# Optimization experiments

Measured on AMD Instinct MI355X. Metric: run time of the kernel, lower is better.

The kernel has to match this reference:

```python
import jax, jax.numpy as jnp
import numpy as np

S, B, V, D, H, G = 60, 256, 50000, 300, 512, 15  # seq, batch, vocab, embed/proj, hidden, grid
DM, DOUT = 1024, 2
MLP_IN = G * G + 7  # 225 pooled + 7 extra features = 232


def setup_inputs() -> dict:
    key = jax.random.key(0)
    ks = jax.random.split(key, 16)
    n = lambda k, shp: (jax.random.normal(k, shp, jnp.float32) * 0.02)
    return {
        "embed_table": n(ks[0], (V, D)),
        "proj_W": n(ks[1], (D, D)),
        "proj_b": jnp.zeros((D,), jnp.float32),
        "bn_g": jnp.ones((D,), jnp.float32),
        "bn_b": jnp.zeros((D,), jnp.float32),
        "Wih": n(ks[2], (4 * H, D)),
        "Whh": n(ks[3], (4 * H, H)),
        "bih": jnp.zeros((4 * H,), jnp.float32),
        "bhh": jnp.zeros((4 * H,), jnp.float32),
        "W1": n(ks[4], (DM, MLP_IN)),
        "b1": jnp.zeros((DM,), jnp.float32),
        "g1": jnp.ones((DM,), jnp.float32),
        "be1": jnp.zeros((DM,), jnp.float32),
        "W2": n(ks[5], (DM, DM)),
        "b2": jnp.zeros((DM,), jnp.float32),
        "g2": jnp.ones((DM,), jnp.float32),
        "be2": jnp.zeros((DM,), jnp.float32),
        "W3": n(ks[6], (DOUT, DM)),
        "b3": jnp.zeros((DOUT,), jnp.float32),
        "extra_feats": jax.random.normal(ks[7], (B, 7), jnp.float32),
        "sentence1": jax.random.randint(ks[8], (S, B), 0, V, jnp.int32),
        "sentence2": jax.random.randint(ks[9], (S, B), 0, V, jnp.int32),
    }


def _bn(x, g, b, axes):
    mu = x.mean(axis=axes, keepdims=True)
    var = x.var(axis=axes, keepdims=True)
    return (x - mu) * jax.lax.rsqrt(var + 1e-5) * g + b


def reference(embed_table, proj_W, proj_b, bn_g, bn_b, Wih, Whh, bih, bhh,
              W1, b1, g1, be1, W2, b2, g2, be2, W3, b3,
              extra_feats, sentence1, sentence2):
    def encode(tokens):
        e = embed_table[tokens]                      # [S,B,D] gather
        e = e @ proj_W.T + proj_b                    # Bottle Linear over S*B rows
        e = _bn(e, bn_g, bn_b, (0, 1))               # Bottle BatchNorm over S*B rows

        def step(carry, x):
            h, c = carry
            z = x @ Wih.T + h @ Whh.T + (bih + bhh)  # [B,4H], gate order i,f,g,o
            i, f, g_, o = jnp.split(z, 4, axis=-1)
            c = jax.nn.sigmoid(f) * c + jax.nn.sigmoid(i) * jnp.tanh(g_)
            h = jax.nn.sigmoid(o) * jnp.tanh(c)
            return (h, c), h

        init = (jnp.zeros((B, H), e.dtype), jnp.zeros((B, H), e.dtype))
        _, hs = jax.lax.scan(step, init, e)          # [S,B,H]
        return hs.transpose(1, 0, 2)                 # [B,S,H]

    h1 = encode(sentence1)
    h2 = encode(sentence2)

    # pairwise L2 distance matrix per batch element: [B,S,S]
    sq = (jnp.sum(h1 * h1, -1)[:, :, None]
          + jnp.sum(h2 * h2, -1)[:, None, :]
          - 2.0 * jnp.einsum('bid,bjd->bij', h1, h2))
    dist = jnp.sqrt(jnp.maximum(sq, 0.0) + 1e-12)

    # dynamic 15x15 min-pool (S divisible by G => kernel = S//G)
    k = S // G
    pooled = dist.reshape(B, G, k, G, k).min(axis=(2, 4)).reshape(B, G * G)

    x = jnp.concatenate([pooled, extra_feats], axis=1)  # [B,232]
    x = _bn(jax.nn.relu(x @ W1.T + b1), g1, be1, (0,))
    x = _bn(jax.nn.relu(x @ W2.T + b2), g2, be2, (0,))
    return jax.nn.log_softmax(x @ W3.T + b3, axis=-1)   # [B,2]
```

## Files before the change

### kernel.cpp

```cpp
#include <hip/hip_runtime.h>
#include <hip/hip_bf16.h>

#define S_LEN 60
#define BATCH 256
#define EMB   300
#define EMBP  320
#define HID   512
#define DMLP  1024
#define NROW  (2*S_LEN*BATCH)
#define RPS   (S_LEN*BATCH)

typedef __attribute__((ext_vector_type(8))) short short8v;
typedef __attribute__((ext_vector_type(4))) float f32x4;

static __device__ __forceinline__ float sigf(float x){
  return 1.0f/(1.0f+__expf(-x));
}
static __device__ __forceinline__ float tanh_fast(float x){
  x = fminf(fmaxf(x,-40.0f),40.0f);
  float a = __expf(2.0f*x);
  return (a-1.0f)/(a+1.0f);
}
static __device__ __forceinline__ unsigned short f2b(float v){
  __hip_bfloat16 h = __float2bfloat16(v);
  return *(unsigned short*)&h;
}
static __device__ __forceinline__ float b2f(unsigned short u){
  return __uint_as_float(((unsigned int)u)<<16);
}

__global__ __launch_bounds__(256) void k_conv_weights(
    const float* __restrict__ Wih, const float* __restrict__ Whh,
    const float* __restrict__ bih, const float* __restrict__ bhh,
    const float* __restrict__ projW,
    unsigned short* __restrict__ Wihb, unsigned short* __restrict__ Whhb,
    unsigned short* __restrict__ projWb, float* __restrict__ bsum)
{
  const int tid = blockIdx.x*256 + threadIdx.x;
  const int stride = gridDim.x*256;
  for (int i=tid; i<2048*EMBP; i+=stride){
    int n = i/EMBP, k = i - n*EMBP;
    Wihb[i] = f2b((k<EMB) ? Wih[(size_t)n*EMB + k] : 0.0f);
  }
  for (int i=tid; i<2048*HID; i+=stride) Whhb[i] = f2b(Whh[i]);
  for (int i=tid; i<EMBP*EMBP; i+=stride){
    int n = i/EMBP, k = i - n*EMBP;
    projWb[i] = f2b((n<EMB && k<EMB) ? projW[(size_t)n*EMB + k] : 0.0f);
  }
  for (int i=tid; i<2048; i+=stride) bsum[i] = bih[i]+bhh[i];
}

__global__ __launch_bounds__(512) void k_embed_mfma(
    const float* __restrict__ embed, const unsigned short* __restrict__ projWb,
    const float* __restrict__ projb, const int* __restrict__ s1,
    const int* __restrict__ s2, unsigned short* __restrict__ Pb)
{
  __shared__ __align__(16) unsigned short sA0[64*40];
  __shared__ __align__(16) unsigned short sA1[64*40];
  __shared__ __align__(16) unsigned short sW0[64*40];
  __shared__ __align__(16) unsigned short sW1[64*40];
  __shared__ int stok[64];
  const int m0 = blockIdx.x*64, n0 = blockIdx.y*64;
  const int tid = threadIdx.x;
  if (tid < 64){
    int r = m0 + tid;
    stok[tid] = (r < RPS) ? s1[r] : s2[r-RPS];
  }
  __syncthreads();
  const int lane = tid & 63, w = tid>>6;
  const int wr = w>>2, wc = w&3;
  const bool isA = tid < 256;
  const int srow = (tid&255)>>2, sseg = tid&3;
  const float* Arow = embed + (size_t)stok[srow]*EMB;
  const unsigned short* Wrow = projWb + (size_t)(n0+srow)*EMBP;

  const int ldst = srow*40 + sseg*8;
  const int aoff0 = (wr*32 + (lane&15))*40 + (lane>>4)*8;
  const int aoff1 = aoff0 + 16*40;
  const int woff  = (wc*16 + (lane&15))*40 + (lane>>4)*8;

  f32x4 acc0 = {0.f,0.f,0.f,0.f}, acc1 = {0.f,0.f,0.f,0.f};

  auto loadA = [&](int kk)->uint4 {
    int kb = kk*32 + sseg*8;
    unsigned short t8[8];
    if (kb+7 < EMB){
      float4 f0 = *(const float4*)(Arow + kb);
      float4 f1 = *(const float4*)(Arow + kb + 4);
      t8[0]=f2b(f0.x); t8[1]=f2b(f0.y); t8[2]=f2b(f0.z); t8[3]=f2b(f0.w);
      t8[4]=f2b(f1.x); t8[5]=f2b(f1.y); t8[6]=f2b(f1.z); t8[7]=f2b(f1.w);
    } else {
      #pragma unroll
      for (int jq=0; jq<8; jq++){
        int k = kb+jq;
        t8[jq] = f2b((k<EMB) ? Arow[k] : 0.0f);
      }
    }
    uint4 o;
    o.x = (unsigned)t8[0] | ((unsigned)t8[1]<<16);
    o.y = (unsigned)t8[2] | ((unsigned)t8[3]<<16);
    o.z = (unsigned)t8[4] | ((unsigned)t8[5]<<16);
    o.w = (unsigned)t8[6] | ((unsigned)t8[7]<<16);
    return o;
  };

  if (isA) *(uint4*)(sA0 + ldst) = loadA(0);
  else     *(uint4*)(sW0 + ldst) = *(const uint4*)(Wrow + sseg*8);
  __syncthreads();

  for (int kk=0; kk<10; kk++){
    uint4 nv;
    if (kk < 9){
      if (isA) nv = loadA(kk+1);
      else     nv = *(const uint4*)(Wrow + (kk+1)*32 + sseg*8);
    }
    const unsigned short* A = (kk&1) ? sA1 : sA0;
    const unsigned short* W = (kk&1) ? sW1 : sW0;
    short8v af0 = *(const short8v*)(A + aoff0);
    short8v af1 = *(const short8v*)(A + aoff1);
    short8v wf  = *(const short8v*)(W + woff);
    acc0 = __builtin_amdgcn_mfma_f32_16x16x32_bf16(af0, wf, acc0, 0,0,0);
    acc1 = __builtin_amdgcn_mfma_f32_16x16x32_bf16(af1, wf, acc1, 0,0,0);
    if (kk < 9){
      unsigned short* dst = ((kk&1) ? (isA?sA0:sW0) : (isA?sA1:sW1)) + ldst;
      *(uint4*)dst = nv;
    }
    __syncthreads();
  }

  const int cc = wc*16 + (lane&15);
  const int n = n0 + cc;
  const float bias = (n < EMB) ? projb[n] : 0.0f;
  const bool valid = (n < EMB);
  #pragma unroll
  for (int v=0; v<4; v++){
    int r0 = wr*32 + (lane>>4)*4 + v;
    Pb[(size_t)(m0+r0)*EMBP + n]    = f2b(valid ? acc0[v]+bias : 0.0f);
    Pb[(size_t)(m0+r0+16)*EMBP + n] = f2b(valid ? acc1[v]+bias : 0.0f);
  }
}

__global__ __launch_bounds__(320) void k_bn_partial(const unsigned short* __restrict__ Pb,
    float* __restrict__ ps, float* __restrict__ psq)
{
  const int rb = blockIdx.x, sent = blockIdx.y, t = threadIdx.x;
  if (t >= EMB) return;
  const unsigned short* base = Pb + ((size_t)sent*RPS + (size_t)rb*256)*EMBP;
  float s=0.0f, q=0.0f;
  for (int r=0;r<256;r++){
    float v = b2f(base[(size_t)r*EMBP + t]);
    s += v; q = fmaf(v,v,q);
  }
  ps [(size_t)(sent*60+rb)*EMB + t] = s;
  psq[(size_t)(sent*60+rb)*EMB + t] = q;
}

__global__ __launch_bounds__(320) void k_bn_final(const float* __restrict__ ps,
    const float* __restrict__ psq, const float* __restrict__ g,
    const float* __restrict__ b, float* __restrict__ scale, float* __restrict__ shift)
{
  const int sent = blockIdx.x, t = threadIdx.x;
  if (t >= EMB) return;
  float s=0.0f, q=0.0f;
  for (int i=0;i<60;i++){
    s += ps [(size_t)(sent*60+i)*EMB + t];
    q += psq[(size_t)(sent*60+i)*EMB + t];
  }
  float mean = s * (1.0f/15360.0f);
  float var  = q * (1.0f/15360.0f) - mean*mean;
  float sc = g[t] * rsqrtf(var + 1e-5f);
  scale[sent*EMB+t] = sc;
  shift[sent*EMB+t] = b[t] - mean*sc;
}

__global__ __launch_bounds__(256) void k_bn_apply(unsigned short* __restrict__ Pb,
    const float* __restrict__ scale, const float* __restrict__ shift)
{
  const int r = blockIdx.x*8 + (threadIdx.x>>5);
  const int c0 = threadIdx.x & 31;
  const int sent = (r >= RPS) ? 1 : 0;
  unsigned short* row = Pb + (size_t)r*EMBP;
  for (int c=c0; c<EMB; c+=32){
    float v = b2f(row[c]);
    v = fmaf(v, scale[sent*EMB+c], shift[sent*EMB+c]);
    row[c] = f2b(v);
  }
}

__global__ __launch_bounds__(512) void k_lstm_step(
    const unsigned short* __restrict__ Pb,
    const unsigned short* __restrict__ Wihb,
    const unsigned short* __restrict__ Whhb,
    const float* __restrict__ bsum,
    const unsigned short* __restrict__ Hin,
    unsigned short* __restrict__ Hnext,
    float* __restrict__ cst,
    unsigned short* __restrict__ Hout,
    int tstep)
{
  __shared__ __align__(16) unsigned short smem[4*5120];
  float* zs = (float*)smem;

  const int tid = threadIdx.x;
  const int lane = tid & 63, w = tid >> 6;
  const int wr = w >> 2, wc = w & 3;
  const int j0 = (int)blockIdx.x * 16;
  const int m0 = (int)blockIdx.y * 64;
  const int sent = m0 >> 8;
  const int brow = m0 & 255;

  const int half = tid >> 8;
  const int rs = tid & 255;
  const int srow = rs >> 2, sseg = rs & 3;
  const int kb = half*32 + sseg*8;
  const int ldst = half*2560 + srow*40 + sseg*8;

  const unsigned short* pAx = Pb + ((size_t)((sent*S_LEN + tstep)*BATCH) + brow + srow)*EMBP + kb;
  const unsigned short* pAh = Hin + (size_t)(m0 + srow)*HID + kb;
  const int wn = (srow>>4)*HID + j0 + (srow&15);
  const unsigned short* pWx = Wihb + (size_t)wn*EMBP + kb;
  const unsigned short* pWh = Whhb + (size_t)wn*HID  + kb;

  auto loadA = [&](int c)->uint4 {
    return (c < 5) ? *(const uint4*)(pAx + c*64) : *(const uint4*)(pAh + (c-5)*64);
  };
  auto loadW = [&](int c)->uint4 {
    return (c < 5) ? *(const uint4*)(pWx + c*64) : *(const uint4*)(pWh + (c-5)*64);
  };

  const int aoffB = (wr*32 + (lane&15))*40 + (lane>>4)*8;
  const int woffB = (wc*16 + (lane&15))*40 + (lane>>4)*8;

  f32x4 acc0 = {0.f,0.f,0.f,0.f}, acc1 = {0.f,0.f,0.f,0.f};

  uint4 rA[3], rW[3];
  rA[0] = loadA(0); rW[0] = loadW(0);
  rA[1] = loadA(1); rW[1] = loadW(1);
  rA[2] = loadA(2); rW[2] = loadW(2);
  *(uint4*)(smem + ldst)         = rA[0];
  *(uint4*)(smem + 10240 + ldst) = rW[0];
  __syncthreads();

  #pragma unroll
  for (int kk = 0; kk < 13; kk++){
    if (kk + 3 < 13){
      rA[(kk+3)%3] = loadA(kk+3);
      rW[(kk+3)%3] = loadW(kk+3);
    }
    const unsigned short* A = smem + (kk&1)*5120;
    const unsigned short* W = smem + 10240 + (kk&1)*5120;
    #pragma unroll
    for (int h2 = 0; h2 < 2; h2++){
      const int bh = h2*2560;
      short8v wf = *(const short8v*)(W + bh + woffB);
      short8v a0 = *(const short8v*)(A + bh + aoffB);
      short8v a1 = *(const short8v*)(A + bh + aoffB + 16*40);
      acc0 = __builtin_amdgcn_mfma_f32_16x16x32_bf16(a0, wf, acc0, 0,0,0);
      acc1 = __builtin_amdgcn_mfma_f32_16x16x32_bf16(a1, wf, acc1, 0,0,0);
    }
    if (kk + 1 < 13){
      *(uint4*)(smem + ((kk+1)&1)*5120 + ldst)         = rA[(kk+1)%3];
      *(uint4*)(smem + 10240 + ((kk+1)&1)*5120 + ldst) = rW[(kk+1)%3];
    }
    __syncthreads();
  }

  #pragma unroll
  for (int v = 0; v < 4; v++){
    int r0 = wr*32 + (lane>>4)*4 + v;
    int cc = wc*16 + (lane&15);
    zs[r0*66 + cc]      = acc0[v];
    zs[(r0+16)*66 + cc] = acc1[v];
  }
  __syncthreads();

  const int row_e = tid >> 4, jj = tid & 15, j = j0 + jj;
  const float zb0 = bsum[0*HID+j], zb1 = bsum[1*HID+j];
  const float zb2 = bsum[2*HID+j], zb3 = bsum[3*HID+j];
  #pragma unroll
  for (int q = 0; q < 2; q++){
    int row = row_e + q*32;
    int r = m0 + row;
    float zi = zs[row*66 + jj]    + zb0;
    float zf = zs[row*66 + 16+jj] + zb1;
    float zg = zs[row*66 + 32+jj] + zb2;
    float zo = zs[row*66 + 48+jj] + zb3;
    size_t ci = (size_t)r*HID + j;
    float cn = fmaf(sigf(zf), cst[ci], sigf(zi)*tanh_fast(zg));
    cst[ci] = cn;
    float hn = sigf(zo)*tanh_fast(cn);
    unsigned short hb = f2b(hn);
    Hnext[ci] = hb;
    Hout[((size_t)((sent*S_LEN + tstep)*BATCH) + (r&255))*HID + j] = hb;
  }
}

#define SDU 258
__global__ __launch_bounds__(256) void k_dist_pool(
    const unsigned short* __restrict__ Hout, float* __restrict__ pooled)
{
  __shared__ unsigned int h1s[S_LEN*SDU];
  __shared__ unsigned int h2s[S_LEN*SDU];
  __shared__ float n1s[S_LEN], n2s[S_LEN];
  const int b = blockIdx.x, tid = threadIdx.x;
  const unsigned int* H = (const unsigned int*)Hout;
  for (int e=tid; e<S_LEN*256; e+=256){
    int row = e>>8, cu = e&255;
    h1s[row*SDU+cu] = H[((size_t)(0*S_LEN+row)*BATCH + b)*256 + cu];
    h2s[row*SDU+cu] = H[((size_t)(1*S_LEN+row)*BATCH + b)*256 + cu];
  }
  __syncthreads();
  if (tid < S_LEN){
    const unsigned int* rp = &h1s[tid*SDU];
    float q=0.0f;
    for (int cu=0;cu<256;cu++){
      unsigned int u = rp[cu];
      float lo = __uint_as_float(u<<16);
      float hi = __uint_as_float(u & 0xffff0000u);
      q = fmaf(lo,lo,q); q = fmaf(hi,hi,q);
    }
    n1s[tid] = q;
  } else if (tid >= 64 && tid < 64+S_LEN){
    const unsigned int* rp = &h2s[(tid-64)*SDU];
    float q=0.0f;
    for (int cu=0;cu<256;cu++){
      unsigned int u = rp[cu];
      float lo = __uint_as_float(u<<16);
      float hi = __uint_as_float(u & 0xffff0000u);
      q = fmaf(lo,lo,q); q = fmaf(hi,hi,q);
    }
    n2s[tid-64] = q;
  }
  __syncthreads();
  if (tid < 225){
    const int gi = tid/15, gj = tid%15;
    float acc[4][4];
    #pragma unroll
    for (int a=0;a<4;a++)
      #pragma unroll
      for (int c=0;c<4;c++) acc[a][c]=0.0f;
    const unsigned int* r1[4]; const unsigned int* r2[4];
    #pragma unroll
    for (int a=0;a<4;a++){ r1[a]=&h1s[(gi*4+a)*SDU]; r2[a]=&h2s[(gj*4+a)*SDU]; }
    for (int cu=0;cu<256;cu++){
      float lo1[4],hi1[4],lo2[4],hi2[4];
      #pragma unroll
      for (int a=0;a<4;a++){
        unsigned int u = r1[a][cu];
        lo1[a]=__uint_as_float(u<<16); hi1[a]=__uint_as_float(u&0xffff0000u);
      }
      #pragma unroll
      for (int c=0;c<4;c++){
        unsigned int u = r2[c][cu];
        lo2[c]=__uint_as_float(u<<16); hi2[c]=__uint_as_float(u&0xffff0000u);
      }
      #pragma unroll
      for (int a=0;a<4;a++)
        #pragma unroll
        for (int c=0;c<4;c++)
          acc[a][c] = fmaf(lo1[a],lo2[c], fmaf(hi1[a],hi2[c], acc[a][c]));
    }
    float mn = 3.4e38f;
    #pragma unroll
    for (int a=0;a<4;a++)
      #pragma unroll
      for (int c=0;c<4;c++){
        float sq = n1s[gi*4+a] + n2s[gj*4+c] - 2.0f*acc[a][c];
        mn = fminf(mn, sqrtf(fmaxf(sq,0.0f)+1e-12f));
      }
    pooled[(size_t)b*225 + tid] = mn;
  }
}

__global__ __launch_bounds__(256) void k_mlp1(const float* __restrict__ pooled,
    const float* __restrict__ extra, const float* __restrict__ W1,
    const float* __restrict__ b1, float* __restrict__ y1)
{
  __shared__ __align__(16) float xs[232];
  const int b = blockIdx.x, tid = threadIdx.x;
  if (tid < 225) xs[tid] = pooled[(size_t)b*225 + tid];
  else if (tid < 232) xs[tid] = extra[(size_t)b*7 + (tid-225)];
  __syncthreads();
  #pragma unroll
  for (int q=0;q<4;q++){
    int n = tid + q*256;
    float acc = b1[n];
    const float4* wr = (const float4*)(W1 + (size_t)n*232);
    const float4* xr = (const float4*)xs;
    for (int k4=0;k4<58;k4++){
      float4 w = wr[k4]; float4 x = xr[k4];
      acc = fmaf(w.x,x.x, fmaf(w.y,x.y, fmaf(w.z,x.z, fmaf(w.w,x.w, acc))));
    }
    y1[(size_t)b*DMLP + n] = fmaxf(acc, 0.0f);
  }
}

__global__ __launch_bounds__(256) void k_mlp_bn(const float* __restrict__ y,
    const float* __restrict__ g, const float* __restrict__ be,
    float* __restrict__ scale, float* __restrict__ shift)
{
  const int n = blockIdx.x*256 + threadIdx.x;
  float s=0.0f, q=0.0f;
  for (int b=0;b<BATCH;b++){
    float v = y[(size_t)b*DMLP + n];
    s += v; q = fmaf(v,v,q);
  }
  float mean = s * (1.0f/256.0f);
  float var  = q * (1.0f/256.0f) - mean*mean;
  float sc = g[n] * rsqrtf(var + 1e-5f);
  scale[n] = sc;
  shift[n] = be[n] - mean*sc;
}

__global__ __launch_bounds__(256) void k_mlp2(const float* __restrict__ y1,
    const float* __restrict__ scale1, const float* __restrict__ shift1,
    const float* __restrict__ W2, const float* __restrict__ b2,
    float* __restrict__ y2)
{
  __shared__ __align__(16) float xs[4][DMLP];
  const int b0 = blockIdx.x*4, tid = threadIdx.x;
  for (int e=tid; e<4*DMLP; e+=256){
    int bb = e>>10, k = e&1023;
    xs[bb][k] = fmaf(y1[(size_t)(b0+bb)*DMLP + k], scale1[k], shift1[k]);
  }
  __syncthreads();
  #pragma unroll
  for (int q=0;q<4;q++){
    int n = tid + q*256;
    float a0=0.0f,a1=0.0f,a2=0.0f,a3=0.0f;
    const float4* wr = (const float4*)(W2 + (size_t)n*DMLP);
    for (int k4=0;k4<256;k4++){
      float4 w = wr[k4];
      float4 x0 = ((const float4*)xs[0])[k4];
      float4 x1 = ((const float4*)xs[1])[k4];
      float4 x2 = ((const float4*)xs[2])[k4];
      float4 x3 = ((const float4*)xs[3])[k4];
      a0 = fmaf(w.x,x0.x, fmaf(w.y,x0.y, fmaf(w.z,x0.z, fmaf(w.w,x0.w, a0))));
      a1 = fmaf(w.x,x1.x, fmaf(w.y,x1.y, fmaf(w.z,x1.z, fmaf(w.w,x1.w, a1))));
      a2 = fmaf(w.x,x2.x, fmaf(w.y,x2.y, fmaf(w.z,x2.z, fmaf(w.w,x2.w, a2))));
      a3 = fmaf(w.x,x3.x, fmaf(w.y,x3.y, fmaf(w.z,x3.z, fmaf(w.w,x3.w, a3))));
    }
    float bias = b2[n];
    y2[(size_t)(b0+0)*DMLP + n] = fmaxf(a0+bias, 0.0f);
    y2[(size_t)(b0+1)*DMLP + n] = fmaxf(a1+bias, 0.0f);
    y2[(size_t)(b0+2)*DMLP + n] = fmaxf(a2+bias, 0.0f);
    y2[(size_t)(b0+3)*DMLP + n] = fmaxf(a3+bias, 0.0f);
  }
}

__global__ __launch_bounds__(256) void k_mlp3(const float* __restrict__ y2,
    const float* __restrict__ scale2, const float* __restrict__ shift2,
    const float* __restrict__ W3, const float* __restrict__ b3,
    float* __restrict__ out)
{
  __shared__ float r0[256], r1[256];
  const int b = blockIdx.x, tid = threadIdx.x;
  float p0=0.0f, p1=0.0f;
  #pragma unroll
  for (int q=0;q<4;q++){
    int k = tid + q*256;
    float x = fmaf(y2[(size_t)b*DMLP + k], scale2[k], shift2[k]);
    p0 = fmaf(x, W3[k], p0);
    p1 = fmaf(x, W3[DMLP+k], p1);
  }
  r0[tid]=p0; r1[tid]=p1;
  __syncthreads();
  for (int s=128; s>0; s>>=1){
    if (tid<s){ r0[tid]+=r0[tid+s]; r1[tid]+=r1[tid+s]; }
    __syncthreads();
  }
  if (tid==0){
    float l0 = r0[0]+b3[0], l1 = r1[0]+b3[1];
    float m = fmaxf(l0,l1);
    float lse = m + logf(__expf(l0-m)+__expf(l1-m));
    out[b*2+0] = l0-lse;
    out[b*2+1] = l1-lse;
  }
}

extern "C" void kernel_launch(void* const* d_in, const int* in_sizes, int n_in,
                              void* d_out, int out_size, void* d_ws, size_t ws_size,
                              hipStream_t stream)
{
  (void)in_sizes; (void)n_in; (void)out_size; (void)ws_size;
  const float* embed = (const float*)d_in[0];
  const float* projW = (const float*)d_in[1];
  const float* projb = (const float*)d_in[2];
  const float* bn_g  = (const float*)d_in[3];
  const float* bn_b  = (const float*)d_in[4];
  const float* Wih   = (const float*)d_in[5];
  const float* Whh   = (const float*)d_in[6];
  const float* bih   = (const float*)d_in[7];
  const float* bhh   = (const float*)d_in[8];
  const float* W1    = (const float*)d_in[9];
  const float* b1    = (const float*)d_in[10];
  const float* g1    = (const float*)d_in[11];
  const float* be1   = (const float*)d_in[12];
  const float* W2    = (const float*)d_in[13];
  const float* b2    = (const float*)d_in[14];
  const float* g2    = (const float*)d_in[15];
  const float* be2   = (const float*)d_in[16];
  const float* W3    = (const float*)d_in[17];
  const float* b3    = (const float*)d_in[18];
  const float* extra = (const float*)d_in[19];
  const int*   s1    = (const int*)d_in[20];
  const int*   s2    = (const int*)d_in[21];
  float* out = (float*)d_out;

  float* ws = (float*)d_ws;
  size_t off = 0;
  float* ps   = ws + off; off += (size_t)2*60*EMB;
  float* psq  = ws + off; off += (size_t)2*60*EMB;
  float* bnsc = ws + off; off += 2*EMB;
  float* bnsh = ws + off; off += 2*EMB;
  float* bsum = ws + off; off += 2048;
  unsigned short* Pb     = (unsigned short*)(ws + off); off += (size_t)NROW*EMBP/2;
  unsigned short* Wihb   = (unsigned short*)(ws + off); off += (size_t)2048*EMBP/2;
  unsigned short* Whhb   = (unsigned short*)(ws + off); off += (size_t)2048*HID/2;
  unsigned short* projWb = (unsigned short*)(ws + off); off += (size_t)EMBP*EMBP/2;
  float* cst = ws + off; off += (size_t)512*HID;
  unsigned short* Hb0 = (unsigned short*)(ws + off); off += (size_t)512*HID/2;
  unsigned short* Hb1 = (unsigned short*)(ws + off); off += (size_t)512*HID/2;
  unsigned short* Hout = (unsigned short*)(ws + off); off += (size_t)2*S_LEN*BATCH*HID/2;
  float* pooled = ws + off; off += (size_t)BATCH*225;
  float* y1     = ws + off; off += (size_t)BATCH*DMLP;
  float* y2     = ws + off; off += (size_t)BATCH*DMLP;
  float* sc1    = ws + off; off += DMLP;
  float* sh1    = ws + off; off += DMLP;
  float* sc2    = ws + off; off += DMLP;
  float* sh2    = ws + off; off += DMLP;

  hipMemsetAsync(cst, 0, (size_t)(512*HID)*sizeof(float) + (size_t)(512*HID)*sizeof(unsigned short), stream);

  k_conv_weights<<<512, 256, 0, stream>>>(Wih, Whh, bih, bhh, projW,
                                          Wihb, Whhb, projWb, bsum);
  k_embed_mfma<<<dim3(NROW/64, 5), 512, 0, stream>>>(embed, projWb, projb, s1, s2, Pb);
  k_bn_partial<<<dim3(60,2), 320, 0, stream>>>(Pb, ps, psq);
  k_bn_final<<<2, 320, 0, stream>>>(ps, psq, bn_g, bn_b, bnsc, bnsh);
  k_bn_apply<<<NROW/8, 256, 0, stream>>>(Pb, bnsc, bnsh);

  for (int t=0; t<S_LEN; t++){
    const unsigned short* hin = (t & 1) ? Hb1 : Hb0;
    unsigned short*      hnxt = (t & 1) ? Hb0 : Hb1;
    k_lstm_step<<<dim3(32,8), 512, 0, stream>>>(Pb, Wihb, Whhb, bsum,
                                                hin, hnxt, cst, Hout, t);
  }

  k_dist_pool<<<BATCH, 256, 0, stream>>>(Hout, pooled);
  k_mlp1<<<BATCH, 256, 0, stream>>>(pooled, extra, W1, b1, y1);
  k_mlp_bn<<<DMLP/256, 256, 0, stream>>>(y1, g1, be1, sc1, sh1);
  k_mlp2<<<BATCH/4, 256, 0, stream>>>(y1, sc1, sh1, W2, b2, y2);
  k_mlp_bn<<<DMLP/256, 256, 0, stream>>>(y2, g2, be2, sc2, sh2);
  k_mlp3<<<BATCH, 256, 0, stream>>>(y2, sc2, sh2, W3, b3, out);
}
```

Baseline: 1.007 ms.

## Tile MLP layer-2 GEMM with split-K and parallelize BN statistics

```diff
diff --git a/kernel.cpp b/kernel.cpp
--- a/kernel.cpp
+++ b/kernel.cpp
@@ -395,57 +395,102 @@
   }
 }
 
-__global__ __launch_bounds__(256) void k_mlp_bn(const float* __restrict__ y,
+__global__ __launch_bounds__(256) void k_mlp_bn2(const float* __restrict__ y,
     const float* __restrict__ g, const float* __restrict__ be,
     float* __restrict__ scale, float* __restrict__ shift)
 {
-  const int n = blockIdx.x*256 + threadIdx.x;
+  __shared__ float sred[256], qred[256];
+  const int c0 = blockIdx.x*64;
+  const int ch = threadIdx.x & 63, grp = threadIdx.x >> 6;
+  const int n = c0 + ch;
   float s=0.0f, q=0.0f;
-  for (int b=0;b<BATCH;b++){
+  for (int b=grp*64; b<grp*64+64; b++){
     float v = y[(size_t)b*DMLP + n];
     s += v; q = fmaf(v,v,q);
   }
-  float mean = s * (1.0f/256.0f);
-  float var  = q * (1.0f/256.0f) - mean*mean;
-  float sc = g[n] * rsqrtf(var + 1e-5f);
-  scale[n] = sc;
-  shift[n] = be[n] - mean*sc;
-}
-
-__global__ __launch_bounds__(256) void k_mlp2(const float* __restrict__ y1,
-    const float* __restrict__ scale1, const float* __restrict__ shift1,
-    const float* __restrict__ W2, const float* __restrict__ b2,
+  sred[threadIdx.x]=s; qred[threadIdx.x]=q;
+  __syncthreads();
+  if (grp==0){
+    s = sred[ch] + sred[64+ch] + sred[128+ch] + sred[192+ch];
+    q = qred[ch] + qred[64+ch] + qred[128+ch] + qred[192+ch];
+    float mean = s * (1.0f/256.0f);
+    float var  = q * (1.0f/256.0f) - mean*mean;
+    float sc = g[n] * rsqrtf(var + 1e-5f);
+    scale[n] = sc;
+    shift[n] = be[n] - mean*sc;
+  }
+}
+
+__global__ __launch_bounds__(256) void k_mlp2_gemm(
+    const float* __restrict__ y1, const float* __restrict__ scale1,
+    const float* __restrict__ shift1, const float* __restrict__ W2,
+    float* __restrict__ y2part)
+{
+  __shared__ float As[64][33];
+  __shared__ float Bs[64][33];
+  const int n0 = blockIdx.x*64, m0 = blockIdx.y*64;
+  const int kbase = blockIdx.z*256;
+  const int tid = threadIdx.x;
+  const int tx = tid & 15, ty = tid >> 4;
+  float acc[4][4];
+  #pragma unroll
+  for (int a=0;a<4;a++)
+    #pragma unroll
+    for (int b=0;b<4;b++) acc[a][b]=0.0f;
+
+  for (int k0=0; k0<256; k0+=32){
+    #pragma unroll
+    for (int i=0;i<8;i++){
+      int e = tid + i*256;
+      int rl = e>>5, kl = e&31;
+      int kk = kbase + k0 + kl;
+      As[rl][kl] = fmaf(y1[(size_t)(m0+rl)*DMLP + kk], scale1[kk], shift1[kk]);
+      Bs[rl][kl] = W2[(size_t)(n0+rl)*DMLP + kk];
+    }
+    __syncthreads();
+    #pragma unroll
+    for (int kk=0;kk<32;kk++){
+      float a[4], w[4];
+      #pragma unroll
+      for (int rl=0;rl<4;rl++) a[rl] = As[ty*4+rl][kk];
+      #pragma unroll
+      for (int cj=0;cj<4;cj++) w[cj] = Bs[cj*16+tx][kk];
+      #pragma unroll
+      for (int rl=0;rl<4;rl++)
+        #pragma unroll
+        for (int cj=0;cj<4;cj++) acc[rl][cj] = fmaf(a[rl], w[cj], acc[rl][cj]);
+    }
+    __syncthreads();
+  }
+  float* dst = y2part + ((size_t)blockIdx.z*BATCH)*DMLP;
+  #pragma unroll
+  for (int rl=0;rl<4;rl++){
+    int r = m0 + ty*4 + rl;
+    #pragma unroll
+    for (int cj=0;cj<4;cj++){
+      int n = n0 + cj*16 + tx;
+      dst[(size_t)r*DMLP + n] = acc[rl][cj];
+    }
+  }
+}
+
+__global__ __launch_bounds__(256) void k_mlp2_fin(
+    const float* __restrict__ y2part, const float* __restrict__ b2,
     float* __restrict__ y2)
 {
-  __shared__ __align__(16) float xs[4][DMLP];
-  const int b0 = blockIdx.x*4, tid = threadIdx.x;
-  for (int e=tid; e<4*DMLP; e+=256){
-    int bb = e>>10, k = e&1023;
-    xs[bb][k] = fmaf(y1[(size_t)(b0+bb)*DMLP + k], scale1[k], shift1[k]);
-  }
-  __syncthreads();
-  #pragma unroll
-  for (int q=0;q<4;q++){
-    int n = tid + q*256;
-    float a0=0.0f,a1=0.0f,a2=0.0f,a3=0.0f;
-    const float4* wr = (const float4*)(W2 + (size_t)n*DMLP);
-    for (int k4=0;k4<256;k4++){
-      float4 w = wr[k4];
-      float4 x0 = ((const float4*)xs[0])[k4];
-      float4 x1 = ((const float4*)xs[1])[k4];
-      float4 x2 = ((const float4*)xs[2])[k4];
-      float4 x3 = ((const float4*)xs[3])[k4];
-      a0 = fmaf(w.x,x0.x, fmaf(w.y,x0.y, fmaf(w.z,x0.z, fmaf(w.w,x0.w, a0))));
-      a1 = fmaf(w.x,x1.x, fmaf(w.y,x1.y, fmaf(w.z,x1.z, fmaf(w.w,x1.w, a1))));
-      a2 = fmaf(w.x,x2.x, fmaf(w.y,x2.y, fmaf(w.z,x2.z, fmaf(w.w,x2.w, a2))));
-      a3 = fmaf(w.x,x3.x, fmaf(w.y,x3.y, fmaf(w.z,x3.z, fmaf(w.w,x3.w, a3))));
-    }
-    float bias = b2[n];
-    y2[(size_t)(b0+0)*DMLP + n] = fmaxf(a0+bias, 0.0f);
-    y2[(size_t)(b0+1)*DMLP + n] = fmaxf(a1+bias, 0.0f);
-    y2[(size_t)(b0+2)*DMLP + n] = fmaxf(a2+bias, 0.0f);
-    y2[(size_t)(b0+3)*DMLP + n] = fmaxf(a3+bias, 0.0f);
-  }
+  const int b = blockIdx.x;
+  const int n = threadIdx.x*4;
+  float4 p0 = *(const float4*)(y2part + ((size_t)(0*BATCH + b))*DMLP + n);
+  float4 p1 = *(const float4*)(y2part + ((size_t)(1*BATCH + b))*DMLP + n);
+  float4 p2 = *(const float4*)(y2part + ((size_t)(2*BATCH + b))*DMLP + n);
+  float4 p3 = *(const float4*)(y2part + ((size_t)(3*BATCH + b))*DMLP + n);
+  float4 bb = *(const float4*)(b2 + n);
+  float4 o;
+  o.x = fmaxf(p0.x+p1.x+p2.x+p3.x+bb.x, 0.0f);
+  o.y = fmaxf(p0.y+p1.y+p2.y+p3.y+bb.y, 0.0f);
+  o.z = fmaxf(p0.z+p1.z+p2.z+p3.z+bb.z, 0.0f);
+  o.w = fmaxf(p0.w+p1.w+p2.w+p3.w+bb.w, 0.0f);
+  *(float4*)(y2 + (size_t)b*DMLP + n) = o;
 }
 
 __global__ __launch_bounds__(256) void k_mlp3(const float* __restrict__ y2,
@@ -525,6 +570,7 @@
   float* pooled = ws + off; off += (size_t)BATCH*225;
   float* y1     = ws + off; off += (size_t)BATCH*DMLP;
   float* y2     = ws + off; off += (size_t)BATCH*DMLP;
+  float* y2part = ws + off; off += (size_t)4*BATCH*DMLP;
   float* sc1    = ws + off; off += DMLP;
   float* sh1    = ws + off; off += DMLP;
   float* sc2    = ws + off; off += DMLP;
@@ -548,8 +594,9 @@
 
   k_dist_pool<<<BATCH, 256, 0, stream>>>(Hout, pooled);
   k_mlp1<<<BATCH, 256, 0, stream>>>(pooled, extra, W1, b1, y1);
-  k_mlp_bn<<<DMLP/256, 256, 0, stream>>>(y1, g1, be1, sc1, sh1);
-  k_mlp2<<<BATCH/4, 256, 0, stream>>>(y1, sc1, sh1, W2, b2, y2);
-  k_mlp_bn<<<DMLP/256, 256, 0, stream>>>(y2, g2, be2, sc2, sh2);
+  k_mlp_bn2<<<16, 256, 0, stream>>>(y1, g1, be1, sc1, sh1);
+  k_mlp2_gemm<<<dim3(16,4,4), 256, 0, stream>>>(y1, sc1, sh1, W2, y2part);
+  k_mlp2_fin<<<BATCH, 256, 0, stream>>>(y2part, b2, y2);
+  k_mlp_bn2<<<16, 256, 0, stream>>>(y2, g2, be2, sc2, sh2);
   k_mlp3<<<BATCH, 256, 0, stream>>>(y2, sc2, sh2, W3, b3, out);
 }
```

Measured after the change: 879.0 us. 12.7% less time.
